# Kernel tuning notes

Measured on AMD Instinct MI355X. Metric: run time of the kernel, lower is better.

## Reference

```python
import jax, jax.numpy as jnp
import numpy as np

D_MODEL = 1024
N_HEADS = 16
HEAD_DIM = D_MODEL // N_HEADS


def setup_inputs() -> dict:
    key = jax.random.key(0)
    k1, k2, k3 = jax.random.split(key, 3)
    B, T = 4, 2048
    x = jax.random.normal(k1, (B, T, D_MODEL), dtype=jnp.float32)
    # match nn.Linear default init scale roughly (small weights for stability)
    w_qkv = jax.random.normal(k2, (D_MODEL, 3 * D_MODEL), dtype=jnp.float32) / np.sqrt(D_MODEL)
    w_proj = jax.random.normal(k3, (D_MODEL, D_MODEL), dtype=jnp.float32) / np.sqrt(D_MODEL)
    b_proj = jnp.zeros((D_MODEL,), dtype=jnp.float32)
    return {"x": x, "w_qkv": w_qkv, "w_proj": w_proj, "b_proj": b_proj}


def reference(x, w_qkv, w_proj, b_proj):
    B, T, C = x.shape
    qkv = x @ w_qkv  # [B,T,3C]
    q, k, v = jnp.split(qkv, 3, axis=-1)
    # [B, H, T, hd]
    q = q.reshape(B, T, N_HEADS, HEAD_DIM).transpose(0, 2, 1, 3)
    k = k.reshape(B, T, N_HEADS, HEAD_DIM).transpose(0, 2, 1, 3)
    v = v.reshape(B, T, N_HEADS, HEAD_DIM).transpose(0, 2, 1, 3)
    scale = 1.0 / np.sqrt(HEAD_DIM).astype(np.float32)
    att = jnp.einsum("bhqd,bhkd->bhqk", q, k) * scale
    causal = jnp.tril(jnp.ones((T, T), dtype=bool))
    att = jnp.where(causal[None, None], att, jnp.float32(-jnp.inf))
    att = jax.nn.softmax(att, axis=-1)
    # dropout p=0.0 (eval) -> identity
    out = jnp.einsum("bhqk,bhkd->bhqd", att, v)
    out = out.transpose(0, 2, 1, 3).reshape(B, T, C)
    return out @ w_proj + b_proj
```

## Files before the change

### kernel.cpp

```cpp
#include <hip/hip_runtime.h>
#include <stdint.h>

#define D_MODEL 1024
#define N_HEADS 16
#define HEAD_DIM 64
#define BATCH 4
#define SEQ 2048
#define ROWS (BATCH * SEQ)
#define K3 (3 * D_MODEL)
#define NQT (SEQ / 64)
#define SCALE_Q 0.1803368867f

typedef unsigned short u16;
typedef unsigned int u32;
typedef __attribute__((ext_vector_type(8))) short short8;
typedef __attribute__((ext_vector_type(4))) float floatx4;

typedef const __attribute__((address_space(1))) u32* gptr_t;
typedef __attribute__((address_space(3))) u32* lptr_t;

__device__ __forceinline__ unsigned cvt_pk(float lo, float hi) {
    unsigned r;
    asm("v_cvt_pk_bf16_f32 %0, %1, %2" : "=v"(r) : "v"(lo), "v"(hi));
    return r;
}

__global__ __launch_bounds__(256) void prep_fused(const float* __restrict__ x,
                                                  u16* __restrict__ xb,
                                                  const float* __restrict__ w_qkv,
                                                  u16* __restrict__ wt_qkv,
                                                  const float* __restrict__ w_proj,
                                                  u16* __restrict__ wt_proj) {
    __shared__ u16 tile[64][65];
    const int bid = blockIdx.x;
    if (bid < 8192) {
        const int i = bid * 256 + threadIdx.x;
        float4 v = ((const float4*)x)[i];
        uint2 p;
        p.x = cvt_pk(v.x, v.y);
        p.y = cvt_pk(v.z, v.w);
        ((uint2*)xb)[i] = p;
        return;
    }
    const float* w;
    u16* wt;
    int C, bx, by;
    if (bid < 8192 + 768) {
        const int r = bid - 8192;
        w = w_qkv; wt = wt_qkv; C = K3;
        bx = r % 48; by = r / 48;
    } else {
        const int r = bid - 8960;
        w = w_proj; wt = wt_proj; C = D_MODEL;
        bx = r & 15; by = r >> 4;
    }
    const int R = D_MODEL;
    const int tx = threadIdx.x & 63;
    const int ty = threadIdx.x >> 6;
    const int r0 = by * 64, c0 = bx * 64;
    #pragma unroll
    for (int i = 0; i < 16; i += 2) {
        const float a = w[(size_t)(r0 + i * 4 + ty) * C + c0 + tx];
        const float b = w[(size_t)(r0 + (i + 1) * 4 + ty) * C + c0 + tx];
        const unsigned p = cvt_pk(a, b);
        tile[i * 4 + ty][tx] = (u16)p;
        tile[(i + 1) * 4 + ty][tx] = (u16)(p >> 16);
    }
    __syncthreads();
    #pragma unroll
    for (int i = 0; i < 16; ++i) {
        const int c = i * 4 + ty;
        wt[(size_t)(c0 + c) * R + r0 + tx] = tile[tx][c];
    }
}

__global__ __launch_bounds__(256) void transpose_v2(const u16* __restrict__ v,
                                                    u16* __restrict__ vt) {
    __shared__ u16 tile[64][65];
    const int bh = blockIdx.y;
    const int t0 = blockIdx.x * 64;
    const int tx = threadIdx.x & 63, ty = threadIdx.x >> 6;
    const u16* src = v + ((size_t)bh * SEQ + t0) * HEAD_DIM;
    #pragma unroll
    for (int i = 0; i < 16; ++i) {
        const int r = i * 4 + ty;
        tile[r][tx] = src[r * HEAD_DIM + tx];
    }
    __syncthreads();
    u16* dst = vt + (size_t)bh * HEAD_DIM * SEQ + t0;
    #pragma unroll
    for (int i = 0; i < 16; ++i) {
        const int d = i * 4 + ty;
        dst[(size_t)d * SEQ + tx] = tile[tx][d];
    }
}

#define PIPE_ISSUE8(buf, k0)                                                   \
    _Pragma("unroll")                                                          \
    for (int i = 0; i < 4; ++i) {                                              \
        const int rb = i * 32 + wave * 8;                                      \
        __builtin_amdgcn_global_load_lds(                                      \
            (gptr_t)(Ab + (size_t)(rb + lrow8) * D_MODEL + (k0)),              \
            (lptr_t)(&As[buf][rb][0]), 16, 0, 0);                              \
        __builtin_amdgcn_global_load_lds(                                      \
            (gptr_t)(Bb + (size_t)(rb + lrow8) * D_MODEL + (k0)),              \
            (lptr_t)(&Bs[buf][rb][0]), 16, 0, 0);                              \
    }

#define PIPE_COMPUTE(buf)                                                      \
    _Pragma("unroll")                                                          \
    for (int ks = 0; ks < 2; ++ks) {                                           \
        const int kk = ks * 32 + quad * 8;                                     \
        short8 af[4], bf[4];                                                   \
        _Pragma("unroll")                                                      \
        for (int t2 = 0; t2 < 4; ++t2) {                                       \
            af[t2] = *(const short8*)&As[buf][wr * 64 + t2 * 16 + l15][kk ^ swA]; \
            bf[t2] = *(const short8*)&Bs[buf][wc * 64 + t2 * 16 + l15][kk ^ swA]; \
        }                                                                      \
        _Pragma("unroll")                                                      \
        for (int i = 0; i < 4; ++i)                                            \
            _Pragma("unroll")                                                  \
            for (int j = 0; j < 4; ++j)                                        \
                acc[i][j] = __builtin_amdgcn_mfma_f32_16x16x32_bf16(           \
                    af[i], bf[j], acc[i][j], 0, 0, 0);                         \
    }

#define WAITV8 do { asm volatile("s_waitcnt vmcnt(8)" ::: "memory");           \
                    __builtin_amdgcn_sched_barrier(0); } while (0)
#define WAITV0 do { asm volatile("s_waitcnt vmcnt(0)" ::: "memory");           \
                    __builtin_amdgcn_sched_barrier(0); } while (0)
#define BARR   do { __builtin_amdgcn_s_barrier();                              \
                    __builtin_amdgcn_sched_barrier(0); } while (0)

#define GEMM_PIPE(NXB)                                                         \
    __shared__ u16 As[2][128][64];                                             \
    __shared__ u16 Bs[2][128][64];                                             \
    const int tid  = threadIdx.x;                                              \
    const int wave = tid >> 6, lane = tid & 63;                                \
    const int quad = lane >> 4, l15 = lane & 15;                               \
    const int wr = wave >> 1, wc = wave & 1;                                   \
    const int bid = (int)(blockIdx.y * gridDim.x + blockIdx.x);                \
    const int nwg = (int)(gridDim.x * gridDim.y);                              \
    const int swz = (bid & 7) * (nwg >> 3) + (bid >> 3);      \
    const int m0 = (swz / (NXB)) * 128, n0 = (swz % (NXB)) * 128;              \
    const int lrow8 = lane >> 3;                                               \
    const int csw = 8 * ((lane & 7) ^ lrow8);           \
    const int swA = (l15 & 7) * 8;                      \
    floatx4 acc[4][4] = {};                                                    \
    const u16* Ab = A  + (size_t)m0 * D_MODEL + csw;                           \
    const u16* Bb = Bt + (size_t)n0 * D_MODEL + csw;                           \
    PIPE_ISSUE8(0, 0)                                                          \
    _Pragma("unroll 1")                                                        \
    for (int t = 0; t < 14; t += 2) {                                          \
        PIPE_ISSUE8(1, (t + 1) * 64)                                           \
        WAITV8; BARR;                                                          \
        PIPE_COMPUTE(0)                                                        \
        BARR;                                                                  \
        PIPE_ISSUE8(0, (t + 2) * 64)                                           \
        WAITV8; BARR;                                                          \
        PIPE_COMPUTE(1)                                                        \
        BARR;                                                                  \
    }                                                                          \
    PIPE_ISSUE8(1, 15 * 64)                                                    \
    WAITV8; BARR;                                                              \
    PIPE_COMPUTE(0)                                                            \
    BARR;                                                                      \
    WAITV0; BARR;                                                              \
    PIPE_COMPUTE(1)

__global__ __launch_bounds__(256) void gemm_qkv(const u16* __restrict__ A,
                                                const u16* __restrict__ Bt,
                                                u16* __restrict__ qo,
                                                u16* __restrict__ ko,
                                                u16* __restrict__ vo) {
    GEMM_PIPE(24)
    const int which = n0 >> 10;
    u16* dst = which == 0 ? qo : (which == 1 ? ko : vo);
    const float scl = which == 0 ? SCALE_Q : 1.f;
    #pragma unroll
    for (int i = 0; i < 4; ++i)
        #pragma unroll
        for (int j = 0; j < 4; ++j) {
            const int col = n0 + wc * 64 + j * 16 + l15;
            const int rb  = m0 + wr * 64 + i * 16 + quad * 4;
            const int cc  = col & 1023;
            const int h = cc >> 6, d = cc & 63;
            #pragma unroll
            for (int rr = 0; rr < 4; rr += 2) {
                const unsigned pw = cvt_pk(acc[i][j][rr] * scl,
                                           acc[i][j][rr + 1] * scl);
                int row = rb + rr;
                int b_ = row >> 11, t_ = row & 2047;
                dst[(((size_t)(b_ * N_HEADS + h)) * SEQ + t_) * HEAD_DIM + d] =
                    (u16)pw;
                row = rb + rr + 1;
                b_ = row >> 11; t_ = row & 2047;
                dst[(((size_t)(b_ * N_HEADS + h)) * SEQ + t_) * HEAD_DIM + d] =
                    (u16)(pw >> 16);
            }
        }
}

__global__ __launch_bounds__(256) void gemm_proj(const u16* __restrict__ A,
                                                 const u16* __restrict__ Bt,
                                                 const float* __restrict__ bias,
                                                 float* __restrict__ out) {
    GEMM_PIPE(8)
    #pragma unroll
    for (int i = 0; i < 4; ++i)
        #pragma unroll
        for (int j = 0; j < 4; ++j) {
            const int col = n0 + wc * 64 + j * 16 + l15;
            const int rb  = m0 + wr * 64 + i * 16 + quad * 4;
            const float bv = bias[col];
            #pragma unroll
            for (int rr = 0; rr < 4; ++rr) {
                const int row = rb + rr;
                out[(size_t)row * D_MODEL + col] = acc[i][j][rr] + bv;
            }
        }
}

__global__ __launch_bounds__(256, 4) void attn_mfma(const u16* __restrict__ q,
                                                    const u16* __restrict__ k,
                                                    const u16* __restrict__ vt,
                                                    u16* __restrict__ o) {
    __shared__ u16 Ks[2][64][64];
    __shared__ u16 Vs[2][64][64];
    __shared__ u16 Plds[4][16][64];
    const int tid = threadIdx.x;
    const int w = tid >> 6, lane = tid & 63;
    const int quad = lane >> 4, l15 = lane & 15;
    const int bid = (int)(blockIdx.y * 16 + blockIdx.x);
    const int swzb = (bid & 7) * 128 + (bid >> 3);
    const int bh = swzb >> 4;
    const int qx = swzb & 15;
    const int b = bh >> 4, h = bh & 15;
    const u16* kb  = k  + (size_t)bh * SEQ * HEAD_DIM;
    const u16* vtb = vt + (size_t)bh * HEAD_DIM * SEQ;
    const int lrow8 = lane >> 3;
    const int csw = 8 * ((lane & 7) ^ lrow8);
    const int swA = (l15 & 7) * 8;
    const int r0 = w * 16 + lrow8;
    const short8 ones = {0x3F80, 0x3F80, 0x3F80, 0x3F80,
                         0x3F80, 0x3F80, 0x3F80, 0x3F80};

    #pragma unroll 1
    for (int seg = 0; seg < 2; ++seg) {
        const int qt = seg ? qx : (NQT - 1 - qx);
        const int qrow = qt * 64 + w * 16 + l15;
        const u16* qp = q + ((size_t)bh * SEQ + qrow) * HEAD_DIM + quad * 8;
        const short8 bq0 = *(const short8*)(qp);
        const short8 bq1 = *(const short8*)(qp + 32);

        floatx4 O[4] = {};
        floatx4 Lacc = {};

        __syncthreads();
        __builtin_amdgcn_global_load_lds(
            (gptr_t)(kb + (size_t)(r0) * HEAD_DIM + csw),
            (lptr_t)(&Ks[0][w * 16][0]), 16, 0, 0);
        __builtin_amdgcn_global_load_lds(
            (gptr_t)(kb + (size_t)(r0 + 8) * HEAD_DIM + csw),
            (lptr_t)(&Ks[0][w * 16 + 8][0]), 16, 0, 0);
        __builtin_amdgcn_global_load_lds(
            (gptr_t)(vtb + (size_t)(r0) * SEQ + csw),
            (lptr_t)(&Vs[0][w * 16][0]), 16, 0, 0);
        __builtin_amdgcn_global_load_lds(
            (gptr_t)(vtb + (size_t)(r0 + 8) * SEQ + csw),
            (lptr_t)(&Vs[0][w * 16 + 8][0]), 16, 0, 0);

        for (int c = 0; c <= qt; ++c) {
            const int cb = c & 1;
            __syncthreads();
            if (c < qt) {
                const int nb = cb ^ 1;
                __builtin_amdgcn_global_load_lds(
                    (gptr_t)(kb + (size_t)((c + 1) * 64 + r0) * HEAD_DIM + csw),
                    (lptr_t)(&Ks[nb][w * 16][0]), 16, 0, 0);
                __builtin_amdgcn_global_load_lds(
                    (gptr_t)(kb + (size_t)((c + 1) * 64 + r0 + 8) * HEAD_DIM + csw),
                    (lptr_t)(&Ks[nb][w * 16 + 8][0]), 16, 0, 0);
                __builtin_amdgcn_global_load_lds(
                    (gptr_t)(vtb + (size_t)(r0) * SEQ + (c + 1) * 64 + csw),
                    (lptr_t)(&Vs[nb][w * 16][0]), 16, 0, 0);
                __builtin_amdgcn_global_load_lds(
                    (gptr_t)(vtb + (size_t)(r0 + 8) * SEQ + (c + 1) * 64 + csw),
                    (lptr_t)(&Vs[nb][w * 16 + 8][0]), 16, 0, 0);
            }
            floatx4 s[4];
            #pragma unroll
            for (int kt = 0; kt < 4; ++kt) {
                short8 ak0 = *(const short8*)&Ks[cb][kt * 16 + l15][(quad * 8) ^ swA];
                short8 ak1 = *(const short8*)&Ks[cb][kt * 16 + l15][(32 + quad * 8) ^ swA];
                floatx4 z = {};
                z = __builtin_amdgcn_mfma_f32_16x16x32_bf16(ak0, bq0, z, 0, 0, 0);
                z = __builtin_amdgcn_mfma_f32_16x16x32_bf16(ak1, bq1, z, 0, 0, 0);
                s[kt] = z;
            }
            float e[4][4];
            #pragma unroll
            for (int kt = 0; kt < 4; ++kt)
                #pragma unroll
                for (int r = 0; r < 4; ++r)
                    e[kt][r] = exp2f(s[kt][r]);
            if (c == qt) {
                #pragma unroll
                for (int kt = 0; kt < 4; ++kt)
                    #pragma unroll
                    for (int r = 0; r < 4; ++r)
                        if (kt * 16 + quad * 4 + r > w * 16 + l15) e[kt][r] = 0.f;
            }
            #pragma unroll
            for (int kt = 0; kt < 4; ++kt) {
                uint2 pkv;
                pkv.x = cvt_pk(e[kt][0], e[kt][1]);
                pkv.y = cvt_pk(e[kt][2], e[kt][3]);
                *(uint2*)&Plds[w][l15][(kt * 16 + quad * 4) ^ swA] = pkv;
            }
            short8 pb0 = *(const short8*)&Plds[w][l15][(quad * 8) ^ swA];
            short8 pb1 = *(const short8*)&Plds[w][l15][(32 + quad * 8) ^ swA];
            #pragma unroll
            for (int dt = 0; dt < 4; ++dt) {
                short8 av0 = *(const short8*)&Vs[cb][dt * 16 + l15][(quad * 8) ^ swA];
                short8 av1 = *(const short8*)&Vs[cb][dt * 16 + l15][(32 + quad * 8) ^ swA];
                O[dt] = __builtin_amdgcn_mfma_f32_16x16x32_bf16(av0, pb0, O[dt], 0, 0, 0);
                O[dt] = __builtin_amdgcn_mfma_f32_16x16x32_bf16(av1, pb1, O[dt], 0, 0, 0);
            }
            Lacc = __builtin_amdgcn_mfma_f32_16x16x32_bf16(ones, pb0, Lacc, 0, 0, 0);
            Lacc = __builtin_amdgcn_mfma_f32_16x16x32_bf16(ones, pb1, Lacc, 0, 0, 0);
        }
        const float inv = 1.f / Lacc[0];
        u16* op = o + ((size_t)(b * SEQ + qrow)) * D_MODEL + h * 64 + quad * 4;
        #pragma unroll
        for (int dt = 0; dt < 4; ++dt) {
            uint2 pkv;
            pkv.x = cvt_pk(O[dt][0] * inv, O[dt][1] * inv);
            pkv.y = cvt_pk(O[dt][2] * inv, O[dt][3] * inv);
            *(uint2*)(op + dt * 16) = pkv;
        }
    }
}

extern "C" void kernel_launch(void* const* d_in, const int* in_sizes, int n_in,
                              void* d_out, int out_size, void* d_ws, size_t ws_size,
                              hipStream_t stream) {
    const float* x      = (const float*)d_in[0];
    const float* w_qkv  = (const float*)d_in[1];
    const float* w_proj = (const float*)d_in[2];
    const float* b_proj = (const float*)d_in[3];
    float* out = (float*)d_out;

    u16* xb      = (u16*)d_ws;
    u16* wt_qkv  = xb + (size_t)ROWS * D_MODEL;
    u16* wt_proj = wt_qkv + (size_t)D_MODEL * K3;
    u16* qws     = wt_proj + (size_t)D_MODEL * D_MODEL;
    u16* kws     = qws + (size_t)ROWS * D_MODEL;
    u16* vtws    = kws + (size_t)ROWS * D_MODEL;
    u16* aout    = vtws + (size_t)ROWS * D_MODEL;
    u16* vnat    = aout;

    prep_fused<<<8192 + 768 + 256, 256, 0, stream>>>(x, xb, w_qkv, wt_qkv,
                                                     w_proj, wt_proj);

    gemm_qkv<<<dim3(K3 / 128, ROWS / 128), 256, 0, stream>>>(xb, wt_qkv, qws, kws, vnat);

    transpose_v2<<<dim3(SEQ / 64, BATCH * N_HEADS), 256, 0, stream>>>(vnat, vtws);

    attn_mfma<<<dim3(NQT / 2, BATCH * N_HEADS), 256, 0, stream>>>(qws, kws, vtws, aout);

    gemm_proj<<<dim3(D_MODEL / 128, ROWS / 128), 256, 0, stream>>>(aout, wt_proj, b_proj, out);
}
```

Before: 241.4 us.

## Split attention into one q-tile per block and single-buffer V with mid-iteration wait

The attention kernel now launches one block per 64-row query tile instead of pairing a long and short tile per block, ordered longest-first. V is single-buffered and its load is issued at the start of each iteration, then waited on with an explicit vmcnt and barrier just before the PV MFMAs, so it overlaps the QK and softmax work. The saved LDS allows raising the occupancy hint to 5 blocks per CU. The trade-offs are less balanced per-block work, since causal tiles vary in length, and V load latency that is no longer hidden a full iteration ahead.

```diff
diff --git a/kernel.cpp b/kernel.cpp
--- a/kernel.cpp
+++ b/kernel.cpp
@@ -221,20 +221,20 @@
         }
 }
 
-__global__ __launch_bounds__(256, 4) void attn_mfma(const u16* __restrict__ q,
+__global__ __launch_bounds__(256, 5) void attn_mfma(const u16* __restrict__ q,
                                                     const u16* __restrict__ k,
                                                     const u16* __restrict__ vt,
                                                     u16* __restrict__ o) {
     __shared__ u16 Ks[2][64][64];
-    __shared__ u16 Vs[2][64][64];
+    __shared__ u16 Vs[64][64];
     __shared__ u16 Plds[4][16][64];
     const int tid = threadIdx.x;
     const int w = tid >> 6, lane = tid & 63;
     const int quad = lane >> 4, l15 = lane & 15;
-    const int bid = (int)(blockIdx.y * 16 + blockIdx.x);
-    const int swzb = (bid & 7) * 128 + (bid >> 3);
-    const int bh = swzb >> 4;
-    const int qx = swzb & 15;
+    const int bid = (int)(blockIdx.y * 32 + blockIdx.x);
+    const int swzb = (bid & 7) * 256 + (bid >> 3);
+    const int bh = swzb >> 5;
+    const int qt = NQT - 1 - (swzb & 31);
     const int b = bh >> 4, h = bh & 15;
     const u16* kb  = k  + (size_t)bh * SEQ * HEAD_DIM;
     const u16* vtb = vt + (size_t)bh * HEAD_DIM * SEQ;
@@ -245,100 +245,97 @@
     const short8 ones = {0x3F80, 0x3F80, 0x3F80, 0x3F80,
                          0x3F80, 0x3F80, 0x3F80, 0x3F80};
 
-    #pragma unroll 1
-    for (int seg = 0; seg < 2; ++seg) {
-        const int qt = seg ? qx : (NQT - 1 - qx);
-        const int qrow = qt * 64 + w * 16 + l15;
-        const u16* qp = q + ((size_t)bh * SEQ + qrow) * HEAD_DIM + quad * 8;
-        const short8 bq0 = *(const short8*)(qp);
-        const short8 bq1 = *(const short8*)(qp + 32);
-
-        floatx4 O[4] = {};
-        floatx4 Lacc = {};
-
+    const int qrow = qt * 64 + w * 16 + l15;
+    const u16* qp = q + ((size_t)bh * SEQ + qrow) * HEAD_DIM + quad * 8;
+    const short8 bq0 = *(const short8*)(qp);
+    const short8 bq1 = *(const short8*)(qp + 32);
+
+    floatx4 O[4] = {};
+    floatx4 Lacc = {};
+
+    __builtin_amdgcn_global_load_lds(
+        (gptr_t)(kb + (size_t)(r0) * HEAD_DIM + csw),
+        (lptr_t)(&Ks[0][w * 16][0]), 16, 0, 0);
+    __builtin_amdgcn_global_load_lds(
+        (gptr_t)(kb + (size_t)(r0 + 8) * HEAD_DIM + csw),
+        (lptr_t)(&Ks[0][w * 16 + 8][0]), 16, 0, 0);
+
+    for (int c = 0; c <= qt; ++c) {
+        const int cb = c & 1;
         __syncthreads();
         __builtin_amdgcn_global_load_lds(
-            (gptr_t)(kb + (size_t)(r0) * HEAD_DIM + csw),
-            (lptr_t)(&Ks[0][w * 16][0]), 16, 0, 0);
+            (gptr_t)(vtb + (size_t)(r0) * SEQ + c * 64 + csw),
+            (lptr_t)(&Vs[w * 16][0]), 16, 0, 0);
         __builtin_amdgcn_global_load_lds(
-            (gptr_t)(kb + (size_t)(r0 + 8) * HEAD_DIM + csw),
-            (lptr_t)(&Ks[0][w * 16 + 8][0]), 16, 0, 0);
-        __builtin_amdgcn_global_load_lds(
-            (gptr_t)(vtb + (size_t)(r0) * SEQ + csw),
-            (lptr_t)(&Vs[0][w * 16][0]), 16, 0, 0);
-        __builtin_amdgcn_global_load_lds(
-            (gptr_t)(vtb + (size_t)(r0 + 8) * SEQ + csw),
-            (lptr_t)(&Vs[0][w * 16 + 8][0]), 16, 0, 0);
-
-        for (int c = 0; c <= qt; ++c) {
-            const int cb = c & 1;
-            __syncthreads();
-            if (c < qt) {
-                const int nb = cb ^ 1;
-                __builtin_amdgcn_global_load_lds(
-                    (gptr_t)(kb + (size_t)((c + 1) * 64 + r0) * HEAD_DIM + csw),
-                    (lptr_t)(&Ks[nb][w * 16][0]), 16, 0, 0);
-                __builtin_amdgcn_global_load_lds(
-                    (gptr_t)(kb + (size_t)((c + 1) * 64 + r0 + 8) * HEAD_DIM + csw),
-                    (lptr_t)(&Ks[nb][w * 16 + 8][0]), 16, 0, 0);
-                __builtin_amdgcn_global_load_lds(
-                    (gptr_t)(vtb + (size_t)(r0) * SEQ + (c + 1) * 64 + csw),
-                    (lptr_t)(&Vs[nb][w * 16][0]), 16, 0, 0);
-                __builtin_amdgcn_global_load_lds(
-                    (gptr_t)(vtb + (size_t)(r0 + 8) * SEQ + (c + 1) * 64 + csw),
-                    (lptr_t)(&Vs[nb][w * 16 + 8][0]), 16, 0, 0);
-            }
-            floatx4 s[4];
+            (gptr_t)(vtb + (size_t)(r0 + 8) * SEQ + c * 64 + csw),
+            (lptr_t)(&Vs[w * 16 + 8][0]), 16, 0, 0);
+        if (c < qt) {
+            const int nb = cb ^ 1;
+            __builtin_amdgcn_global_load_lds(
+                (gptr_t)(kb + (size_t)((c + 1) * 64 + r0) * HEAD_DIM + csw),
+                (lptr_t)(&Ks[nb][w * 16][0]), 16, 0, 0);
+            __builtin_amdgcn_global_load_lds(
+                (gptr_t)(kb + (size_t)((c + 1) * 64 + r0 + 8) * HEAD_DIM + csw),
+                (lptr_t)(&Ks[nb][w * 16 + 8][0]), 16, 0, 0);
+        }
+        floatx4 s[4];
+        #pragma unroll
+        for (int kt = 0; kt < 4; ++kt) {
+            short8 ak0 = *(const short8*)&Ks[cb][kt * 16 + l15][(quad * 8) ^ swA];
+            short8 ak1 = *(const short8*)&Ks[cb][kt * 16 + l15][(32 + quad * 8) ^ swA];
+            floatx4 z = {};
+            z = __builtin_amdgcn_mfma_f32_16x16x32_bf16(ak0, bq0, z, 0, 0, 0);
+            z = __builtin_amdgcn_mfma_f32_16x16x32_bf16(ak1, bq1, z, 0, 0, 0);
+            s[kt] = z;
+        }
+        float e[4][4];
+        #pragma unroll
+        for (int kt = 0; kt < 4; ++kt)
             #pragma unroll
-            for (int kt = 0; kt < 4; ++kt) {
-                short8 ak0 = *(const short8*)&Ks[cb][kt * 16 + l15][(quad * 8) ^ swA];
-                short8 ak1 = *(const short8*)&Ks[cb][kt * 16 + l15][(32 + quad * 8) ^ swA];
-                floatx4 z = {};
-                z = __builtin_amdgcn_mfma_f32_16x16x32_bf16(ak0, bq0, z, 0, 0, 0);
-                z = __builtin_amdgcn_mfma_f32_16x16x32_bf16(ak1, bq1, z, 0, 0, 0);
-                s[kt] = z;
-            }
-            float e[4][4];
+            for (int r = 0; r < 4; ++r)
+                e[kt][r] = exp2f(s[kt][r]);
+        if (c == qt) {
             #pragma unroll
             for (int kt = 0; kt < 4; ++kt)
                 #pragma unroll
                 for (int r = 0; r < 4; ++r)
-                    e[kt][r] = exp2f(s[kt][r]);
-            if (c == qt) {
-                #pragma unroll
-                for (int kt = 0; kt < 4; ++kt)
-                    #pragma unroll
-                    for (int r = 0; r < 4; ++r)
-                        if (kt * 16 + quad * 4 + r > w * 16 + l15) e[kt][r] = 0.f;
-            }
-            #pragma unroll
-            for (int kt = 0; kt < 4; ++kt) {
-                uint2 pkv;
-                pkv.x = cvt_pk(e[kt][0], e[kt][1]);
-                pkv.y = cvt_pk(e[kt][2], e[kt][3]);
-                *(uint2*)&Plds[w][l15][(kt * 16 + quad * 4) ^ swA] = pkv;
-            }
-            short8 pb0 = *(const short8*)&Plds[w][l15][(quad * 8) ^ swA];
-            short8 pb1 = *(const short8*)&Plds[w][l15][(32 + quad * 8) ^ swA];
-            #pragma unroll
-            for (int dt = 0; dt < 4; ++dt) {
-                short8 av0 = *(const short8*)&Vs[cb][dt * 16 + l15][(quad * 8) ^ swA];
-                short8 av1 = *(const short8*)&Vs[cb][dt * 16 + l15][(32 + quad * 8) ^ swA];
-                O[dt] = __builtin_amdgcn_mfma_f32_16x16x32_bf16(av0, pb0, O[dt], 0, 0, 0);
-                O[dt] = __builtin_amdgcn_mfma_f32_16x16x32_bf16(av1, pb1, O[dt], 0, 0, 0);
-            }
-            Lacc = __builtin_amdgcn_mfma_f32_16x16x32_bf16(ones, pb0, Lacc, 0, 0, 0);
-            Lacc = __builtin_amdgcn_mfma_f32_16x16x32_bf16(ones, pb1, Lacc, 0, 0, 0);
-        }
-        const float inv = 1.f / Lacc[0];
-        u16* op = o + ((size_t)(b * SEQ + qrow)) * D_MODEL + h * 64 + quad * 4;
+                    if (kt * 16 + quad * 4 + r > w * 16 + l15) e[kt][r] = 0.f;
+        }
+        #pragma unroll
+        for (int kt = 0; kt < 4; ++kt) {
+            uint2 pkv;
+            pkv.x = cvt_pk(e[kt][0], e[kt][1]);
+            pkv.y = cvt_pk(e[kt][2], e[kt][3]);
+            *(uint2*)&Plds[w][l15][(kt * 16 + quad * 4) ^ swA] = pkv;
+        }
+        short8 pb0 = *(const short8*)&Plds[w][l15][(quad * 8) ^ swA];
+        short8 pb1 = *(const short8*)&Plds[w][l15][(32 + quad * 8) ^ swA];
+        if (c < qt) {
+            asm volatile("s_waitcnt vmcnt(2)" ::: "memory");
+        } else {
+            asm volatile("s_waitcnt vmcnt(0)" ::: "memory");
+        }
+        __builtin_amdgcn_sched_barrier(0);
+        __builtin_amdgcn_s_barrier();
+        __builtin_amdgcn_sched_barrier(0);
         #pragma unroll
         for (int dt = 0; dt < 4; ++dt) {
-            uint2 pkv;
-            pkv.x = cvt_pk(O[dt][0] * inv, O[dt][1] * inv);
-            pkv.y = cvt_pk(O[dt][2] * inv, O[dt][3] * inv);
-            *(uint2*)(op + dt * 16) = pkv;
-        }
+            short8 av0 = *(const short8*)&Vs[dt * 16 + l15][(quad * 8) ^ swA];
+            short8 av1 = *(const short8*)&Vs[dt * 16 + l15][(32 + quad * 8) ^ swA];
+            O[dt] = __builtin_amdgcn_mfma_f32_16x16x32_bf16(av0, pb0, O[dt], 0, 0, 0);
+            O[dt] = __builtin_amdgcn_mfma_f32_16x16x32_bf16(av1, pb1, O[dt], 0, 0, 0);
+        }
+        Lacc = __builtin_amdgcn_mfma_f32_16x16x32_bf16(ones, pb0, Lacc, 0, 0, 0);
+        Lacc = __builtin_amdgcn_mfma_f32_16x16x32_bf16(ones, pb1, Lacc, 0, 0, 0);
+    }
+    const float inv = 1.f / Lacc[0];
+    u16* op = o + ((size_t)(b * SEQ + qrow)) * D_MODEL + h * 64 + quad * 4;
+    #pragma unroll
+    for (int dt = 0; dt < 4; ++dt) {
+        uint2 pkv;
+        pkv.x = cvt_pk(O[dt][0] * inv, O[dt][1] * inv);
+        pkv.y = cvt_pk(O[dt][2] * inv, O[dt][3] * inv);
+        *(uint2*)(op + dt * 16) = pkv;
     }
 }
 
@@ -367,7 +364,7 @@
 
     transpose_v2<<<dim3(SEQ / 64, BATCH * N_HEADS), 256, 0, stream>>>(vnat, vtws);
 
-    attn_mfma<<<dim3(NQT / 2, BATCH * N_HEADS), 256, 0, stream>>>(qws, kws, vtws, aout);
+    attn_mfma<<<dim3(NQT, BATCH * N_HEADS), 256, 0, stream>>>(qws, kws, vtws, aout);
 
     gemm_proj<<<dim3(D_MODEL / 128, ROWS / 128), 256, 0, stream>>>(aout, wt_proj, b_proj, out);
 }
```

Measured after the change: 257.8 us. 6.8% more time.

## Process two adjacent query tiles per block sharing each K/V chunk load

Applied to the files above, without the earlier changes.

Each attention block used to handle two query tiles on opposite ends of the causal range in turn, which balanced work but loaded the K/V tiles twice. It now handles two adjacent 64-row query tiles, 2pj and 2pj+1, in one pass over the key chunks. Each K/V chunk staged in LDS is reused by both tiles, with separate causal masks on the last two chunks. This halves K/V global traffic and barriers per unit of work, but blocks now carry uneven amounts of work. The heaviest block's critical path is roughly twice as long as before, and it holds more registers for the two accumulator sets.

```diff
diff --git a/kernel.cpp b/kernel.cpp
--- a/kernel.cpp
+++ b/kernel.cpp
@@ -234,7 +234,8 @@
     const int bid = (int)(blockIdx.y * 16 + blockIdx.x);
     const int swzb = (bid & 7) * 128 + (bid >> 3);
     const int bh = swzb >> 4;
-    const int qx = swzb & 15;
+    const int pj = 15 - (swzb & 15);
+    const int QT = 2 * pj + 1;
     const int b = bh >> 4, h = bh & 15;
     const u16* kb  = k  + (size_t)bh * SEQ * HEAD_DIM;
     const u16* vtb = vt + (size_t)bh * HEAD_DIM * SEQ;
@@ -245,57 +246,58 @@
     const short8 ones = {0x3F80, 0x3F80, 0x3F80, 0x3F80,
                          0x3F80, 0x3F80, 0x3F80, 0x3F80};
 
-    #pragma unroll 1
-    for (int seg = 0; seg < 2; ++seg) {
-        const int qt = seg ? qx : (NQT - 1 - qx);
-        const int qrow = qt * 64 + w * 16 + l15;
-        const u16* qp = q + ((size_t)bh * SEQ + qrow) * HEAD_DIM + quad * 8;
-        const short8 bq0 = *(const short8*)(qp);
-        const short8 bq1 = *(const short8*)(qp + 32);
-
-        floatx4 O[4] = {};
-        floatx4 Lacc = {};
-
+    const int qrow_a = (2 * pj) * 64 + w * 16 + l15;
+    const int qrow_b = qrow_a + 64;
+    const u16* qpa = q + ((size_t)bh * SEQ + qrow_a) * HEAD_DIM + quad * 8;
+    const u16* qpb = q + ((size_t)bh * SEQ + qrow_b) * HEAD_DIM + quad * 8;
+    const short8 bqa0 = *(const short8*)(qpa);
+    const short8 bqa1 = *(const short8*)(qpa + 32);
+    const short8 bqb0 = *(const short8*)(qpb);
+    const short8 bqb1 = *(const short8*)(qpb + 32);
+
+    floatx4 Oa[4] = {}, Ob[4] = {};
+    floatx4 La = {}, Lb = {};
+
+    __builtin_amdgcn_global_load_lds(
+        (gptr_t)(kb + (size_t)(r0) * HEAD_DIM + csw),
+        (lptr_t)(&Ks[0][w * 16][0]), 16, 0, 0);
+    __builtin_amdgcn_global_load_lds(
+        (gptr_t)(kb + (size_t)(r0 + 8) * HEAD_DIM + csw),
+        (lptr_t)(&Ks[0][w * 16 + 8][0]), 16, 0, 0);
+    __builtin_amdgcn_global_load_lds(
+        (gptr_t)(vtb + (size_t)(r0) * SEQ + csw),
+        (lptr_t)(&Vs[0][w * 16][0]), 16, 0, 0);
+    __builtin_amdgcn_global_load_lds(
+        (gptr_t)(vtb + (size_t)(r0 + 8) * SEQ + csw),
+        (lptr_t)(&Vs[0][w * 16 + 8][0]), 16, 0, 0);
+
+    for (int c = 0; c <= QT; ++c) {
+        const int cb = c & 1;
         __syncthreads();
-        __builtin_amdgcn_global_load_lds(
-            (gptr_t)(kb + (size_t)(r0) * HEAD_DIM + csw),
-            (lptr_t)(&Ks[0][w * 16][0]), 16, 0, 0);
-        __builtin_amdgcn_global_load_lds(
-            (gptr_t)(kb + (size_t)(r0 + 8) * HEAD_DIM + csw),
-            (lptr_t)(&Ks[0][w * 16 + 8][0]), 16, 0, 0);
-        __builtin_amdgcn_global_load_lds(
-            (gptr_t)(vtb + (size_t)(r0) * SEQ + csw),
-            (lptr_t)(&Vs[0][w * 16][0]), 16, 0, 0);
-        __builtin_amdgcn_global_load_lds(
-            (gptr_t)(vtb + (size_t)(r0 + 8) * SEQ + csw),
-            (lptr_t)(&Vs[0][w * 16 + 8][0]), 16, 0, 0);
-
-        for (int c = 0; c <= qt; ++c) {
-            const int cb = c & 1;
-            __syncthreads();
-            if (c < qt) {
-                const int nb = cb ^ 1;
-                __builtin_amdgcn_global_load_lds(
-                    (gptr_t)(kb + (size_t)((c + 1) * 64 + r0) * HEAD_DIM + csw),
-                    (lptr_t)(&Ks[nb][w * 16][0]), 16, 0, 0);
-                __builtin_amdgcn_global_load_lds(
-                    (gptr_t)(kb + (size_t)((c + 1) * 64 + r0 + 8) * HEAD_DIM + csw),
-                    (lptr_t)(&Ks[nb][w * 16 + 8][0]), 16, 0, 0);
-                __builtin_amdgcn_global_load_lds(
-                    (gptr_t)(vtb + (size_t)(r0) * SEQ + (c + 1) * 64 + csw),
-                    (lptr_t)(&Vs[nb][w * 16][0]), 16, 0, 0);
-                __builtin_amdgcn_global_load_lds(
-                    (gptr_t)(vtb + (size_t)(r0 + 8) * SEQ + (c + 1) * 64 + csw),
-                    (lptr_t)(&Vs[nb][w * 16 + 8][0]), 16, 0, 0);
-            }
+        if (c < QT) {
+            const int nb = cb ^ 1;
+            __builtin_amdgcn_global_load_lds(
+                (gptr_t)(kb + (size_t)((c + 1) * 64 + r0) * HEAD_DIM + csw),
+                (lptr_t)(&Ks[nb][w * 16][0]), 16, 0, 0);
+            __builtin_amdgcn_global_load_lds(
+                (gptr_t)(kb + (size_t)((c + 1) * 64 + r0 + 8) * HEAD_DIM + csw),
+                (lptr_t)(&Ks[nb][w * 16 + 8][0]), 16, 0, 0);
+            __builtin_amdgcn_global_load_lds(
+                (gptr_t)(vtb + (size_t)(r0) * SEQ + (c + 1) * 64 + csw),
+                (lptr_t)(&Vs[nb][w * 16][0]), 16, 0, 0);
+            __builtin_amdgcn_global_load_lds(
+                (gptr_t)(vtb + (size_t)(r0 + 8) * SEQ + (c + 1) * 64 + csw),
+                (lptr_t)(&Vs[nb][w * 16 + 8][0]), 16, 0, 0);
+        }
+        if (c < QT) {
             floatx4 s[4];
             #pragma unroll
             for (int kt = 0; kt < 4; ++kt) {
                 short8 ak0 = *(const short8*)&Ks[cb][kt * 16 + l15][(quad * 8) ^ swA];
                 short8 ak1 = *(const short8*)&Ks[cb][kt * 16 + l15][(32 + quad * 8) ^ swA];
                 floatx4 z = {};
-                z = __builtin_amdgcn_mfma_f32_16x16x32_bf16(ak0, bq0, z, 0, 0, 0);
-                z = __builtin_amdgcn_mfma_f32_16x16x32_bf16(ak1, bq1, z, 0, 0, 0);
+                z = __builtin_amdgcn_mfma_f32_16x16x32_bf16(ak0, bqa0, z, 0, 0, 0);
+                z = __builtin_amdgcn_mfma_f32_16x16x32_bf16(ak1, bqa1, z, 0, 0, 0);
                 s[kt] = z;
             }
             float e[4][4];
@@ -304,7 +306,7 @@
                 #pragma unroll
                 for (int r = 0; r < 4; ++r)
                     e[kt][r] = exp2f(s[kt][r]);
-            if (c == qt) {
+            if (c == QT - 1) {
                 #pragma unroll
                 for (int kt = 0; kt < 4; ++kt)
                     #pragma unroll
@@ -324,21 +326,69 @@
             for (int dt = 0; dt < 4; ++dt) {
                 short8 av0 = *(const short8*)&Vs[cb][dt * 16 + l15][(quad * 8) ^ swA];
                 short8 av1 = *(const short8*)&Vs[cb][dt * 16 + l15][(32 + quad * 8) ^ swA];
-                O[dt] = __builtin_amdgcn_mfma_f32_16x16x32_bf16(av0, pb0, O[dt], 0, 0, 0);
-                O[dt] = __builtin_amdgcn_mfma_f32_16x16x32_bf16(av1, pb1, O[dt], 0, 0, 0);
-            }
-            Lacc = __builtin_amdgcn_mfma_f32_16x16x32_bf16(ones, pb0, Lacc, 0, 0, 0);
-            Lacc = __builtin_amdgcn_mfma_f32_16x16x32_bf16(ones, pb1, Lacc, 0, 0, 0);
+                Oa[dt] = __builtin_amdgcn_mfma_f32_16x16x32_bf16(av0, pb0, Oa[dt], 0, 0, 0);
+                Oa[dt] = __builtin_amdgcn_mfma_f32_16x16x32_bf16(av1, pb1, Oa[dt], 0, 0, 0);
+            }
+            La = __builtin_amdgcn_mfma_f32_16x16x32_bf16(ones, pb0, La, 0, 0, 0);
+            La = __builtin_amdgcn_mfma_f32_16x16x32_bf16(ones, pb1, La, 0, 0, 0);
         }
-        const float inv = 1.f / Lacc[0];
-        u16* op = o + ((size_t)(b * SEQ + qrow)) * D_MODEL + h * 64 + quad * 4;
-        #pragma unroll
-        for (int dt = 0; dt < 4; ++dt) {
-            uint2 pkv;
-            pkv.x = cvt_pk(O[dt][0] * inv, O[dt][1] * inv);
-            pkv.y = cvt_pk(O[dt][2] * inv, O[dt][3] * inv);
-            *(uint2*)(op + dt * 16) = pkv;
+        {
+            floatx4 s[4];
+            #pragma unroll
+            for (int kt = 0; kt < 4; ++kt) {
+                short8 ak0 = *(const short8*)&Ks[cb][kt * 16 + l15][(quad * 8) ^ swA];
+                short8 ak1 = *(const short8*)&Ks[cb][kt * 16 + l15][(32 + quad * 8) ^ swA];
+                floatx4 z = {};
+                z = __builtin_amdgcn_mfma_f32_16x16x32_bf16(ak0, bqb0, z, 0, 0, 0);
+                z = __builtin_amdgcn_mfma_f32_16x16x32_bf16(ak1, bqb1, z, 0, 0, 0);
+                s[kt] = z;
+            }
+            float e[4][4];
+            #pragma unroll
+            for (int kt = 0; kt < 4; ++kt)
+                #pragma unroll
+                for (int r = 0; r < 4; ++r)
+                    e[kt][r] = exp2f(s[kt][r]);
+            if (c == QT) {
+                #pragma unroll
+                for (int kt = 0; kt < 4; ++kt)
+                    #pragma unroll
+                    for (int r = 0; r < 4; ++r)
+                        if (kt * 16 + quad * 4 + r > w * 16 + l15) e[kt][r] = 0.f;
+            }
+            #pragma unroll
+            for (int kt = 0; kt < 4; ++kt) {
+                uint2 pkv;
+                pkv.x = cvt_pk(e[kt][0], e[kt][1]);
+                pkv.y = cvt_pk(e[kt][2], e[kt][3]);
+                *(uint2*)&Plds[w][l15][(kt * 16 + quad * 4) ^ swA] = pkv;
+            }
+            short8 pb0 = *(const short8*)&Plds[w][l15][(quad * 8) ^ swA];
+            short8 pb1 = *(const short8*)&Plds[w][l15][(32 + quad * 8) ^ swA];
+            #pragma unroll
+            for (int dt = 0; dt < 4; ++dt) {
+                short8 av0 = *(const short8*)&Vs[cb][dt * 16 + l15][(quad * 8) ^ swA];
+                short8 av1 = *(const short8*)&Vs[cb][dt * 16 + l15][(32 + quad * 8) ^ swA];
+                Ob[dt] = __builtin_amdgcn_mfma_f32_16x16x32_bf16(av0, pb0, Ob[dt], 0, 0, 0);
+                Ob[dt] = __builtin_amdgcn_mfma_f32_16x16x32_bf16(av1, pb1, Ob[dt], 0, 0, 0);
+            }
+            Lb = __builtin_amdgcn_mfma_f32_16x16x32_bf16(ones, pb0, Lb, 0, 0, 0);
+            Lb = __builtin_amdgcn_mfma_f32_16x16x32_bf16(ones, pb1, Lb, 0, 0, 0);
         }
+    }
+    const float inva = 1.f / La[0];
+    const float invb = 1.f / Lb[0];
+    u16* opa = o + ((size_t)(b * SEQ + qrow_a)) * D_MODEL + h * 64 + quad * 4;
+    u16* opb = o + ((size_t)(b * SEQ + qrow_b)) * D_MODEL + h * 64 + quad * 4;
+    #pragma unroll
+    for (int dt = 0; dt < 4; ++dt) {
+        uint2 pa, pb;
+        pa.x = cvt_pk(Oa[dt][0] * inva, Oa[dt][1] * inva);
+        pa.y = cvt_pk(Oa[dt][2] * inva, Oa[dt][3] * inva);
+        pb.x = cvt_pk(Ob[dt][0] * invb, Ob[dt][1] * invb);
+        pb.y = cvt_pk(Ob[dt][2] * invb, Ob[dt][3] * invb);
+        *(uint2*)(opa + dt * 16) = pa;
+        *(uint2*)(opb + dt * 16) = pb;
     }
 }
 
```

Result: slower. 277.6 us (+15.0%).
